# Kernel optimization log

Hardware: AMD Instinct MI355X
Metric: run time of the kernel (lower is better)

## Reference

```python
import jax, jax.numpy as jnp
import numpy as np

NEG_INF = -1e10  # finite stand-in for torch NEG_INF; safe under logaddexp
EOS = 1
BLANK = -1  # blank is the last vocab index (self.blank = -1)


def setup_inputs() -> dict:
    key = jax.random.key(0)
    k1, k2, k3 = jax.random.split(key, 3)
    T, V = 1500, 32000
    N, U = 8, 10
    ctc_beam = 2048
    ctc_prob = jax.random.normal(k1, (T, V), dtype=jnp.float32)
    g = jax.random.randint(k2, (N, U), 0, V)
    c = jax.random.randint(k3, (N * ctc_beam,), 0, V)
    return {"ctc_prob": ctc_prob, "g": g, "c": c}


def reference(ctc_prob, g, c):
    # --- constructor math ---
    logp = jax.nn.log_softmax(ctc_prob, axis=-1)  # T x V
    T, V = logp.shape
    N, U = g.shape
    NB = c.shape[0]
    ctc_beam = NB // N
    blank_lp = logp[:, BLANK]                     # T
    gamma_b_g0 = jnp.cumsum(blank_lp)             # T  (running blank logprob)
    # state after repeat_interleave(beam) along batch dim -> T x NB
    gamma_b_g = jnp.broadcast_to(gamma_b_g0[:, None], (T, NB))
    gamma_n_g = jnp.full((T, NB), NEG_INF, jnp.float32)
    ctc_score0 = jnp.zeros((NB,), jnp.float32)    # ctc_score repeated to NB

    # --- forward ---
    lp_c = logp[:, c]                             # T x NB, gathered per candidate
    glen = U - 1                                  # static
    start = max(glen, 1)
    if glen == 0:
        init_n = lp_c[0]
    else:
        init_n = jnp.full((NB,), NEG_INF, jnp.float32)
    init_b = jnp.full((NB,), NEG_INF, jnp.float32)
    score0 = init_n
    repeat = jnp.repeat(g[:, -1], ctc_beam) != c  # NB bool
    neg = jnp.float32(NEG_INF)

    def step(carry, xs):
        n_prev, b_prev, score = carry
        gb_gm1, gn_gm1, lp_c_t, lp_b_t = xs
        term = jnp.where(repeat, gn_gm1, neg)
        phi = jnp.logaddexp(gb_gm1, term)
        n_t = jnp.logaddexp(n_prev, phi) + lp_c_t
        b_t = jnp.logaddexp(b_prev, n_prev) + lp_b_t
        score = jnp.logaddexp(score, phi + lp_c_t)
        return (n_t, b_t, score), None

    xs = (
        gamma_b_g[start - 1:T - 1],                               # gamma_b_g[t-1]
        gamma_n_g[start - 1:T - 1],                               # gamma_n_g[t-1]
        lp_c[start:],                                             # ctc_prob[t, c]
        jnp.broadcast_to(blank_lp[start:, None], (T - start, NB)),  # ctc_prob[t, blank]
    )
    (_, _, score), _ = jax.lax.scan(step, (init_n, init_b, score0), xs)

    is_eos = c == EOS
    gamma_nb_g = jnp.logaddexp(gamma_b_g[-1], gamma_n_g[-1])
    score = jnp.where(is_eos, gamma_nb_g, score)
    delta_score = (score - ctc_score0).reshape(-1, ctc_beam)  # N x ctc_beam
    return delta_score
```

## Files before the change

kernel.cpp:

```cpp
#include <hip/hip_runtime.h>
#include <hip/hip_fp16.h>

#define T_DIM   1500
#define V4      8000
#define START_T 9
#define NB      16384
#define BLOCK   1024
#define CPT     16
#define NPAIR   8
#define NJ      8
#define TAIL_N  832
#define ROWS    6
#define NCHUNK  250
#define NEGBIG  -3.0e38f
#define EOS_ID  1
#define LN2     0.69314718055994531f
#define L2E     1.44269504088896341f

#if __has_builtin(__builtin_amdgcn_exp2f)
__device__ __forceinline__ float fexp2(float x) { return __builtin_amdgcn_exp2f(x); }
#else
__device__ __forceinline__ float fexp2(float x) { return __expf(x * LN2); }
#endif
#if __has_builtin(__builtin_amdgcn_logf)
__device__ __forceinline__ float flog2(float x) { return __builtin_amdgcn_logf(x); }
#else
__device__ __forceinline__ float flog2(float x) { return __logf(x) * L2E; }
#endif

#define WG_BARRIER() do { \
  asm volatile("s_waitcnt lgkmcnt(0)" ::: "memory"); \
  __builtin_amdgcn_s_barrier(); \
  asm volatile("" ::: "memory"); \
} while (0)

struct alignas(8) H4 { __half2 a, b; };

__global__ __launch_bounds__(BLOCK)
void ctc_k1(const float* __restrict__ P, const int* __restrict__ cidx,
            float* __restrict__ Lws, float* __restrict__ Sblank)
{
  __shared__ __align__(16) __half rowh[2][32768];
  __shared__ float red[2][20];
  const int tid = threadIdx.x;
  const int q   = blockIdx.x;
  const int t0  = q * ROWS;

  unsigned cidp[NPAIR];
  float s[CPT];
#pragma unroll
  for (int j = 0; j < NPAIR; ++j) {
    unsigned c0 = (unsigned)cidx[(2*j  )*BLOCK + tid] * 2u;
    unsigned c1 = (unsigned)cidx[(2*j+1)*BLOCK + tid] * 2u;
    cidp[j] = c0 | (c1 << 16);
    s[2*j] = 0.f; s[2*j+1] = 0.f;
  }

  const float4* __restrict__ P4 = (const float4*)P;
  const bool tailv = (tid < TAIL_N);

  float4 va[NJ], vb[NJ];

  auto LOAD = [&](float4 (&v)[NJ], int t) {
    const float4* rp = P4 + (long)t * V4;
#pragma unroll
    for (int j = 0; j < 7; ++j) v[j] = rp[j*BLOCK + tid];
    v[7] = tailv ? rp[7*BLOCK + tid] : make_float4(NEGBIG, NEGBIG, NEGBIG, NEGBIG);
  };

  auto STAGE = [&](float4 (&v)[NJ], int buf) {
    float ls = 0.f;
    H4* rw = (H4*)rowh[buf];
#pragma unroll
    for (int j = 0; j < NJ; ++j) {
      float p0 = fexp2(v[j].x * L2E);
      float p1 = fexp2(v[j].y * L2E);
      float p2 = fexp2(v[j].z * L2E);
      float p3 = fexp2(v[j].w * L2E);
      ls += (p0 + p1) + (p2 + p3);
      H4 h; h.a = __floats2half2_rn(p0, p1); h.b = __floats2half2_rn(p2, p3);
      rw[j*BLOCK + tid] = h;
    }
#pragma unroll
    for (int d = 1; d < 64; d <<= 1) ls += __shfl_xor(ls, d);
    if ((tid & 63) == 0) red[buf][tid >> 6] = ls;
    if (tid == TAIL_N - 1) red[buf][16] = v[7].w * L2E;
  };

  float Blocal2 = 0.f;
  auto GATHER = [&](int t, int buf) {
    float sum = red[buf][0];
#pragma unroll
    for (int w = 1; w < 16; ++w) sum += red[buf][w];
    const float lse2 = flog2(sum);
    if (t >= START_T) {
      const float sc = fexp2(Blocal2 - lse2);
      const char* rb = (const char*)rowh[buf];
#pragma unroll
      for (int j = 0; j < NPAIR; ++j) {
        unsigned pk = cidp[j];
        float p0 = __half2float(*(const __half*)(rb + (pk & 0xffffu)));
        float p1 = __half2float(*(const __half*)(rb + (pk >> 16)));
        s[2*j]   = fmaf(sc, p0, s[2*j]);
        s[2*j+1] = fmaf(sc, p1, s[2*j+1]);
      }
    }
    Blocal2 += red[buf][16] - lse2;
  };

  LOAD(va, t0 + 0);
  LOAD(vb, t0 + 1);
  STAGE(va, 0);
  WG_BARRIER();

  LOAD(va, t0 + 2);  GATHER(t0 + 0, 0);  STAGE(vb, 1);  WG_BARRIER();
  LOAD(vb, t0 + 3);  GATHER(t0 + 1, 1);  STAGE(va, 0);  WG_BARRIER();
  LOAD(va, t0 + 4);  GATHER(t0 + 2, 0);  STAGE(vb, 1);  WG_BARRIER();
  LOAD(vb, t0 + 5);  GATHER(t0 + 3, 1);  STAGE(va, 0);  WG_BARRIER();
                     GATHER(t0 + 4, 0);  STAGE(vb, 1);  WG_BARRIER();
                     GATHER(t0 + 5, 1);

#pragma unroll
  for (int k = 0; k < CPT; ++k) {
    float L = (s[k] > 0.f) ? flog2(s[k]) * LN2 : NEGBIG;
    Lws[(long)q*NB + k*BLOCK + tid] = L;
  }
  if (tid == 0) Sblank[q] = Blocal2 * LN2;
}

#define K3_BLOCK 256
#define K3_CPB   128

__global__ __launch_bounds__(K3_BLOCK)
void ctc_k3(const float* __restrict__ Lws, const float* __restrict__ Sblank,
            const int* __restrict__ cidx, float* __restrict__ out, int nchunk)
{
  __shared__ float base[258];
  __shared__ float wsum[4];
  __shared__ float redm[K3_BLOCK], reds[K3_BLOCK];
  const int tid = threadIdx.x;

  float orig = (tid < nchunk) ? Sblank[tid] : 0.f;
  float x = orig;
#pragma unroll
  for (int d = 1; d < 64; d <<= 1) {
    float y = __shfl_up(x, d);
    if ((tid & 63) >= d) x += y;
  }
  if ((tid & 63) == 63) wsum[tid >> 6] = x;
  __syncthreads();
  {
    const int w = tid >> 6;
    float pre = 0.f;
    if (w > 0) pre += wsum[0];
    if (w > 1) pre += wsum[1];
    if (w > 2) pre += wsum[2];
    x += pre;
  }
  if (tid < nchunk)      base[tid] = x - orig;
  if (tid == nchunk - 1) base[nchunk] = x;
  __syncthreads();

  const int half = tid >> 7;
  const int cl   = tid & 127;
  const int i    = blockIdx.x * K3_CPB + cl;
  const int hl   = (nchunk + 1) >> 1;
  const int c0   = half * hl;
  int c1 = c0 + hl; if (c1 > nchunk) c1 = nchunk;

  float mm = NEGBIG, ss = 0.f;
#pragma unroll 4
  for (int q2 = c0; q2 < c1; ++q2) {
    float L = Lws[(long)q2*NB + i] + base[q2];
    float nm = fmaxf(mm, L);
    ss = ss*__expf(mm - nm) + __expf(L - nm);
    mm = nm;
  }
  redm[tid] = mm; reds[tid] = ss;
  __syncthreads();
  if (half == 0) {
    float om = redm[tid + 128], os = reds[tid + 128];
    float nm = fmaxf(mm, om);
    ss = ss*__expf(mm - nm) + os*__expf(om - nm);
    mm = nm;
    float sc = mm + __logf(ss);
    out[i] = (cidx[i] == EOS_ID) ? base[nchunk] : sc;
  }
}

extern "C" void kernel_launch(void* const* d_in, const int* in_sizes, int n_in,
                              void* d_out, int out_size, void* d_ws, size_t ws_size,
                              hipStream_t stream)
{
  const float* P    = (const float*)d_in[0];
  const int*   cidx = (const int*)d_in[2];
  float*       out  = (float*)d_out;

  float* Lws    = (float*)d_ws;
  float* Sblank = Lws + (long)NCHUNK * NB;

  ctc_k1<<<dim3(NCHUNK), dim3(BLOCK), 0, stream>>>(P, cidx, Lws, Sblank);
  ctc_k3<<<dim3(NB / K3_CPB), dim3(K3_BLOCK), 0, stream>>>(Lws, Sblank, cidx, out, NCHUNK);
}
```

Baseline: 53.30 us.

## Warp-specialize k1 into producer and consumer waves with LDS flag handoff

```diff
diff --git a/kernel.cpp b/kernel.cpp
--- a/kernel.cpp
+++ b/kernel.cpp
@@ -5,17 +5,16 @@
 #define V4      8000
 #define START_T 9
 #define NB      16384
-#define BLOCK   1024
-#define CPT     16
-#define NPAIR   8
-#define NJ      8
-#define TAIL_N  832
+#define BLOCK   896
+#define NPROD   6
+#define NCONS   8
 #define ROWS    6
 #define NCHUNK  250
 #define NEGBIG  -3.0e38f
 #define EOS_ID  1
 #define LN2     0.69314718055994531f
 #define L2E     1.44269504088896341f
+#define SENT_U  0x7FC00000u
 
 #if __has_builtin(__builtin_amdgcn_exp2f)
 __device__ __forceinline__ float fexp2(float x) { return __builtin_amdgcn_exp2f(x); }
@@ -28,104 +27,110 @@
 __device__ __forceinline__ float flog2(float x) { return __logf(x) * L2E; }
 #endif
 
-#define WG_BARRIER() do { \
-  asm volatile("s_waitcnt lgkmcnt(0)" ::: "memory"); \
-  __builtin_amdgcn_s_barrier(); \
-  asm volatile("" ::: "memory"); \
-} while (0)
-
 struct alignas(8) H4 { __half2 a, b; };
 
-__global__ __launch_bounds__(BLOCK)
+__global__ __launch_bounds__(BLOCK, 4)
 void ctc_k1(const float* __restrict__ P, const int* __restrict__ cidx,
             float* __restrict__ Lws, float* __restrict__ Sblank)
 {
-  __shared__ __align__(16) __half rowh[2][32768];
-  __shared__ float red[2][20];
+  __shared__ __align__(16) __half A[2][32000];
+  __shared__ float flagsL[8];
+  __shared__ float flagsB[8];
+  __shared__ int   cons[8];
   const int tid = threadIdx.x;
+  const int w   = tid >> 6;
+  const int l   = tid & 63;
   const int q   = blockIdx.x;
   const int t0  = q * ROWS;
 
-  unsigned cidp[NPAIR];
-  float s[CPT];
-#pragma unroll
-  for (int j = 0; j < NPAIR; ++j) {
-    unsigned c0 = (unsigned)cidx[(2*j  )*BLOCK + tid] * 2u;
-    unsigned c1 = (unsigned)cidx[(2*j+1)*BLOCK + tid] * 2u;
-    cidp[j] = c0 | (c1 << 16);
-    s[2*j] = 0.f; s[2*j+1] = 0.f;
-  }
-
-  const float4* __restrict__ P4 = (const float4*)P;
-  const bool tailv = (tid < TAIL_N);
-
-  float4 va[NJ], vb[NJ];
-
-  auto LOAD = [&](float4 (&v)[NJ], int t) {
-    const float4* rp = P4 + (long)t * V4;
-#pragma unroll
-    for (int j = 0; j < 7; ++j) v[j] = rp[j*BLOCK + tid];
-    v[7] = tailv ? rp[7*BLOCK + tid] : make_float4(NEGBIG, NEGBIG, NEGBIG, NEGBIG);
-  };
-
-  auto STAGE = [&](float4 (&v)[NJ], int buf) {
-    float ls = 0.f;
-    H4* rw = (H4*)rowh[buf];
-#pragma unroll
-    for (int j = 0; j < NJ; ++j) {
-      float p0 = fexp2(v[j].x * L2E);
-      float p1 = fexp2(v[j].y * L2E);
-      float p2 = fexp2(v[j].z * L2E);
-      float p3 = fexp2(v[j].w * L2E);
-      ls += (p0 + p1) + (p2 + p3);
-      H4 h; h.a = __floats2half2_rn(p0, p1); h.b = __floats2half2_rn(p2, p3);
-      rw[j*BLOCK + tid] = h;
-    }
-#pragma unroll
-    for (int d = 1; d < 64; d <<= 1) ls += __shfl_xor(ls, d);
-    if ((tid & 63) == 0) red[buf][tid >> 6] = ls;
-    if (tid == TAIL_N - 1) red[buf][16] = v[7].w * L2E;
-  };
-
-  float Blocal2 = 0.f;
-  auto GATHER = [&](int t, int buf) {
-    float sum = red[buf][0];
-#pragma unroll
-    for (int w = 1; w < 16; ++w) sum += red[buf][w];
-    const float lse2 = flog2(sum);
-    if (t >= START_T) {
-      const float sc = fexp2(Blocal2 - lse2);
-      const char* rb = (const char*)rowh[buf];
-#pragma unroll
-      for (int j = 0; j < NPAIR; ++j) {
-        unsigned pk = cidp[j];
-        float p0 = __half2float(*(const __half*)(rb + (pk & 0xffffu)));
-        float p1 = __half2float(*(const __half*)(rb + (pk >> 16)));
-        s[2*j]   = fmaf(sc, p0, s[2*j]);
-        s[2*j+1] = fmaf(sc, p1, s[2*j+1]);
+  if (tid < ROWS) { ((unsigned*)flagsL)[tid] = SENT_U; cons[tid] = 0; }
+  __syncthreads();
+
+  if (w < NPROD) {
+    const int p = w;
+    const float4* rp = (const float4*)P + (long)(t0 + p) * V4;
+    __half* Arow = A[p & 1];
+    float4 va[8], vb[8];
+    float psum = 0.f, blankv = 0.f;
+
+    auto LOADB = [&](float4 (&v)[8], int b) {
+      const int cnt = (b == 15) ? 5 : 8;
+#pragma unroll
+      for (int k = 0; k < 8; ++k) if (k < cnt) v[k] = rp[l + 64*(8*b + k)];
+    };
+    auto CONV = [&](float4 (&v)[8], int b) {
+      const int cnt = (b == 15) ? 5 : 8;
+#pragma unroll
+      for (int k = 0; k < 8; ++k) if (k < cnt) {
+        float p0 = fexp2(v[k].x * L2E), p1 = fexp2(v[k].y * L2E);
+        float p2 = fexp2(v[k].z * L2E), p3 = fexp2(v[k].w * L2E);
+        psum += (p0 + p1) + (p2 + p3);
+        H4 h; h.a = __floats2half2_rn(p0, p1); h.b = __floats2half2_rn(p2, p3);
+        ((H4*)Arow)[l + 64*(8*b + k)] = h;
+        if (b == 15 && k == 4 && l == 63) blankv = v[k].w * L2E;
       }
-    }
-    Blocal2 += red[buf][16] - lse2;
-  };
-
-  LOAD(va, t0 + 0);
-  LOAD(vb, t0 + 1);
-  STAGE(va, 0);
-  WG_BARRIER();
-
-  LOAD(va, t0 + 2);  GATHER(t0 + 0, 0);  STAGE(vb, 1);  WG_BARRIER();
-  LOAD(vb, t0 + 3);  GATHER(t0 + 1, 1);  STAGE(va, 0);  WG_BARRIER();
-  LOAD(va, t0 + 4);  GATHER(t0 + 2, 0);  STAGE(vb, 1);  WG_BARRIER();
-  LOAD(vb, t0 + 5);  GATHER(t0 + 3, 1);  STAGE(va, 0);  WG_BARRIER();
-                     GATHER(t0 + 4, 0);  STAGE(vb, 1);  WG_BARRIER();
-                     GATHER(t0 + 5, 1);
-
-#pragma unroll
-  for (int k = 0; k < CPT; ++k) {
-    float L = (s[k] > 0.f) ? flog2(s[k]) * LN2 : NEGBIG;
-    Lws[(long)q*NB + k*BLOCK + tid] = L;
-  }
-  if (tid == 0) Sblank[q] = Blocal2 * LN2;
+    };
+
+    LOADB(va, 0); LOADB(vb, 1);
+    if (p >= 2) {
+      volatile int* cv = cons;
+      while (cv[p - 2] < NCONS) __builtin_amdgcn_s_sleep(2);
+      asm volatile("" ::: "memory");
+    }
+#pragma unroll
+    for (int b = 0; b < 16; b += 2) {
+      CONV(va, b);
+      if (b + 2 < 16) LOADB(va, b + 2);
+      CONV(vb, b + 1);
+      if (b + 3 < 16) LOADB(vb, b + 3);
+    }
+#pragma unroll
+    for (int d = 1; d < 64; d <<= 1) psum += __shfl_xor(psum, d);
+    if (l == 63) flagsB[p] = blankv;
+    asm volatile("s_waitcnt lgkmcnt(0)" ::: "memory");
+    if (l == 0) flagsL[p] = flog2(psum);
+  } else {
+    const int cw = w - NPROD;
+    unsigned cidp[16];
+    float s[32];
+#pragma unroll
+    for (int j = 0; j < 16; ++j) {
+      unsigned c0 = (unsigned)cidx[cw*2048 + (2*j  )*64 + l] * 2u;
+      unsigned c1 = (unsigned)cidx[cw*2048 + (2*j+1)*64 + l] * 2u;
+      cidp[j] = c0 | (c1 << 16);
+      s[2*j] = 0.f; s[2*j+1] = 0.f;
+    }
+    float Bl2 = 0.f;
+    volatile unsigned* fl = (volatile unsigned*)flagsL;
+    volatile float*    fb = (volatile float*)flagsB;
+    for (int r = 0; r < ROWS; ++r) {
+      while (fl[r] == SENT_U) __builtin_amdgcn_s_sleep(2);
+      asm volatile("" ::: "memory");
+      const float lse2 = __uint_as_float(fl[r]);
+      const float b2   = fb[r];
+      if (t0 + r >= START_T) {
+        const float sc = fexp2(Bl2 - lse2);
+        const char* rb = (const char*)A[r & 1];
+#pragma unroll
+        for (int j = 0; j < 16; ++j) {
+          unsigned pk = cidp[j];
+          float p0 = __half2float(*(const __half*)(rb + (pk & 0xffffu)));
+          float p1 = __half2float(*(const __half*)(rb + (pk >> 16)));
+          s[2*j]   = fmaf(sc, p0, s[2*j]);
+          s[2*j+1] = fmaf(sc, p1, s[2*j+1]);
+        }
+      }
+      Bl2 += b2 - lse2;
+      asm volatile("" ::: "memory");
+      if (l == 0) atomicAdd(&cons[r], 1);
+    }
+#pragma unroll
+    for (int k = 0; k < 32; ++k) {
+      float L = (s[k] > 0.f) ? flog2(s[k]) * LN2 : NEGBIG;
+      Lws[(long)q*NB + cw*2048 + k*64 + l] = L;
+    }
+    if (cw == 0 && l == 0) Sblank[q] = Bl2 * LN2;
+  }
 }
 
 #define K3_BLOCK 256
```

New measurement: 53.92 us. No clear change (+1.2%).
